# Performance work log

Measured on AMD Instinct MI355X. Metric: run time of the kernel, lower is better.

## Reference

```python
import jax, jax.numpy as jnp
import numpy as np

B, T, DIN, D = 32, 2048, 512, 512


def setup_inputs() -> dict:
    key = jax.random.key(0)
    k0, k1, k2, k3 = jax.random.split(key, 4)
    x = jax.random.normal(k0, (B, T, DIN), dtype=jnp.float32)
    h0 = jax.random.normal(k1, (B, D), dtype=jnp.float32)
    s0 = jax.random.normal(k2, (B, D), dtype=jnp.float32)
    # nn.Linear(input_dim, 6*hidden_dim): weight [6D, DIN], bias [6D]
    W = jax.random.normal(k3, (6 * D, DIN), dtype=jnp.float32) / np.float32(np.sqrt(DIN))
    b = jnp.zeros((6 * D,), dtype=jnp.float32)
    return {"x": x, "h0": h0, "s0": s0, "W": W, "b": b}


def reference(x, h0, s0, W, b):
    # Fused input projection for all 6 gates, done once as a big GEMM: [B,T,6D]
    proj = jnp.einsum("bti,oi->bto", x, W) + b
    proj = jnp.transpose(proj, (1, 0, 2))  # [T, B, 6D] for scan over time
    sig = jax.nn.sigmoid

    def step(carry, z):
        h, s = carry  # each [B, D]
        z0, z1, z2, z3, z4, z5 = jnp.split(z, 6, axis=-1)
        # gated two-state recurrence (6 gates, input-only projection,
        # elementwise recurrence on h/s as in the fused Triton cell)
        s_new = sig(z0) * s + sig(z1) * jnp.tanh(z2)
        h_new = sig(z3) * h + sig(z4) * jnp.tanh(z5 + s_new)
        return (h_new, s_new), h_new

    (hT, sT), hs = jax.lax.scan(step, (h0, s0), proj)
    out = jnp.transpose(hs, (1, 0, 2))  # [B, T, D]
    return out, sT
```

## Files before the change

kernel.cpp:

```cpp
#include <hip/hip_runtime.h>
#include <hip/hip_bf16.h>
#include <cstddef>
#include <cstdint>

#define BB   32
#define TT   2048
#define DIN  512
#define DD   512
#define NN   3072
#define PW   3072
#define PF   16

#define BMT 256
#define BNT 256
#define BKT 64
#define NKT (DIN / BKT)

typedef __attribute__((ext_vector_type(4))) float f32x4;
typedef __attribute__((ext_vector_type(8))) short s16x8;

__device__ __forceinline__ void gl2lds16(const void* g, void* l) {
    __builtin_amdgcn_global_load_lds(
        (const __attribute__((address_space(1))) unsigned*)g,
        (__attribute__((address_space(3))) unsigned*)l, 16, 0, 0);
}

__device__ __forceinline__ unsigned short bfr(float f) {
    unsigned u = __float_as_uint(f);
    u += 0x7fffu + ((u >> 16) & 1u);
    return (unsigned short)(u >> 16);
}

__device__ __forceinline__ float ftanh(float x) {
    return 1.f - 2.f * __builtin_amdgcn_rcpf(1.f + __builtin_amdgcn_exp2f(x * 2.885390082f));
}

__device__ __forceinline__ float h2lo(unsigned u) {
    return (float)__builtin_bit_cast(_Float16, (unsigned short)(u & 0xffffu));
}
__device__ __forceinline__ float h2hi(unsigned u) {
    return (float)__builtin_bit_cast(_Float16, (unsigned short)(u >> 16));
}

__global__ __launch_bounds__(256) void convert_x(
    const float* __restrict__ x, unsigned short* __restrict__ x2)
{
    const int total4 = BB * TT * DIN / 4;
    for (int idx = blockIdx.x * 256 + threadIdx.x; idx < total4;
         idx += gridDim.x * 256) {
        int e = idx * 4;
        int b = e >> 20;
        int t = (e >> 9) & 2047;
        int i = e & 511;
        float4 v = *(const float4*)(x + (size_t)e);
        ushort4 o;
        o.x = bfr(v.x); o.y = bfr(v.y); o.z = bfr(v.z); o.w = bfr(v.w);
        *(ushort4*)(x2 + ((size_t)((t << 5) | b) << 9) + i) = o;
    }
}

__global__ __launch_bounds__(128) void convert_w(
    const float* __restrict__ W, const float* __restrict__ bias,
    unsigned short* __restrict__ W2, float* __restrict__ bias2)
{
    int c = blockIdx.x;
    int p = c >> 10, d = (c & 1023) >> 1, q = c & 1;
    int o = ((2 * p + q) << 9) + d;
    const float* src = W + (size_t)o * DIN;
    unsigned short* dst = W2 + (size_t)c * DIN;
    int i = threadIdx.x * 4;
    float4 v = *(const float4*)(src + i);
    ushort4 u;
    u.x = bfr(v.x); u.y = bfr(v.y); u.z = bfr(v.z); u.w = bfr(v.w);
    *(ushort4*)(dst + i) = u;
    if (threadIdx.x == 0) bias2[c] = bias[o];
}

__global__ __launch_bounds__(512, 2) void gemm_proj8(
    const unsigned short* __restrict__ x2,
    const unsigned short* __restrict__ W2,
    const float* __restrict__ bias2,
    _Float16* __restrict__ proj,
    int t0)
{
    __shared__ unsigned short lds[4 * 256 * 64];
    unsigned short* const A0 = lds;
    unsigned short* const B0 = lds + 16384;
    unsigned short* const A1 = lds + 32768;
    unsigned short* const B1 = lds + 49152;

    const int tid  = threadIdx.x;
    const int bx   = blockIdx.x % (NN / BNT);
    const int by   = blockIdx.x / (NN / BNT);
    const int row0 = by * BMT;
    const int col0 = bx * BNT;
    const size_t growA = (size_t)t0 * BB + row0;

    const int lane = tid & 63;
    const int wv   = tid >> 6;
    const int wm   = wv >> 2;
    const int wn   = wv & 3;
    const int lr   = lane & 15;
    const int lq   = lane >> 4;

    auto stage = [&](unsigned short* Ab, unsigned short* Bb, int kt) {
        const int k0 = kt * BKT;
        #pragma unroll
        for (int a = 0; a < 4; ++a) {
            int cid = a * 512 + tid;
            int rt  = cid >> 3;
            int cp  = cid & 7;
            int cl  = cp ^ (rt & 7);
            gl2lds16(x2 + (growA + rt) * DIN + k0 + cl * 8, Ab + rt * 64 + cp * 8);
        }
        #pragma unroll
        for (int a = 0; a < 4; ++a) {
            int cid = a * 512 + tid;
            int rt  = cid >> 3;
            int cp  = cid & 7;
            int cl  = cp ^ (rt & 7);
            gl2lds16(W2 + (size_t)(col0 + rt) * DIN + k0 + cl * 8, Bb + rt * 64 + cp * 8);
        }
    };

    f32x4 acc[8][4] = {};

    stage(A0, B0, 0);
    stage(A1, B1, 1);
    asm volatile("s_waitcnt vmcnt(8)" ::: "memory");
    __builtin_amdgcn_s_barrier();

    #pragma unroll
    for (int kt = 0; kt < NKT; ++kt) {
        const unsigned short* Ab = (kt & 1) ? A1 : A0;
        const unsigned short* Bb = (kt & 1) ? B1 : B0;

        s16x8 bv[4][2];
        #pragma unroll
        for (int j = 0; j < 4; ++j) {
            int col = wn * 64 + j * 16 + lr;
            #pragma unroll
            for (int x = 0; x < 2; ++x) {
                int cp = (x * 4 + lq) ^ (col & 7);
                bv[j][x] = *(const s16x8*)(Bb + col * 64 + cp * 8);
            }
        }
        #pragma unroll
        for (int m = 0; m < 8; ++m) {
            int row = wm * 128 + m * 16 + lr;
            s16x8 av0, av1;
            {
                int cp0 = (0 * 4 + lq) ^ (row & 7);
                int cp1 = (1 * 4 + lq) ^ (row & 7);
                av0 = *(const s16x8*)(Ab + row * 64 + cp0 * 8);
                av1 = *(const s16x8*)(Ab + row * 64 + cp1 * 8);
            }
            __builtin_amdgcn_s_setprio(1);
            #pragma unroll
            for (int j = 0; j < 4; ++j) {
                acc[m][j] = __builtin_amdgcn_mfma_f32_16x16x32_bf16(
                    av0, bv[j][0], acc[m][j], 0, 0, 0);
                acc[m][j] = __builtin_amdgcn_mfma_f32_16x16x32_bf16(
                    av1, bv[j][1], acc[m][j], 0, 0, 0);
            }
            __builtin_amdgcn_s_setprio(0);
        }

        __builtin_amdgcn_s_barrier();
        if (kt + 2 < NKT) {
            stage((kt & 1) ? A1 : A0, (kt & 1) ? B1 : B0, kt + 2);
            asm volatile("s_waitcnt vmcnt(8)" ::: "memory");
        } else if (kt + 1 < NKT) {
            asm volatile("s_waitcnt vmcnt(0)" ::: "memory");
        }
        if (kt + 1 < NKT) __builtin_amdgcn_s_barrier();
    }

    #pragma unroll
    for (int j = 0; j < 4; ++j) {
        int col = col0 + wn * 64 + j * 16 + lr;
        int p   = col >> 10;
        int q   = col & 1;
        int k   = 2 * p + q;
        float bc = bias2[col];
        const bool  isT = (k == 2);
        const bool  isI = (k == 5);
        const float m   = isT ? 2.885390082f : -1.442695041f;
        #pragma unroll
        for (int i = 0; i < 8; ++i) {
            int rbase = row0 + wm * 128 + i * 16 + lq * 4;
            #pragma unroll
            for (int r = 0; r < 4; ++r) {
                float z  = acc[i][j][r] + bc;
                float e  = __builtin_amdgcn_exp2f(z * m);
                float rr = __builtin_amdgcn_rcpf(1.f + e);
                float v  = isT ? (1.f - 2.f * rr) : rr;
                if (isI) v = z;
                proj[(size_t)(rbase + r) * PW + col] = (_Float16)v;
            }
        }
    }
}

__global__ __launch_bounds__(64) void scan_chunk(
    const _Float16* __restrict__ proj,
    const float* __restrict__ h0, const float* __restrict__ s0,
    float* __restrict__ outH, float* __restrict__ outS,
    int t0, int Tc)
{
    const int gid = blockIdx.x * 64 + threadIdx.x;
    const int b   = gid >> 9;
    const int d   = gid & 511;

    float h, s;
    if (t0 == 0) { h = h0[gid]; s = s0[gid]; }
    else {
        h = outH[((size_t)b * TT + (t0 - 1)) * DD + d];
        s = outS[gid];
    }

    const unsigned* pu = (const unsigned*)(proj + (size_t)b * PW + d * 2);
    const size_t tstr = (size_t)BB * PW / 2;
    float* oH = outH + ((size_t)b * TT + t0) * DD + d;

    unsigned bufA[PF][3], bufB[PF][3];
    #pragma unroll
    for (int u = 0; u < PF; ++u)
        #pragma unroll
        for (int p = 0; p < 3; ++p)
            bufA[u][p] = pu[(size_t)u * tstr + p * 512];

    for (int tb = 0; tb < Tc; tb += 2 * PF) {
        #pragma unroll
        for (int u = 0; u < PF; ++u) {
            int t = tb + PF + u; if (t > Tc - 1) t = Tc - 1;
            #pragma unroll
            for (int p = 0; p < 3; ++p)
                bufB[u][p] = pu[(size_t)t * tstr + p * 512];
        }
        #pragma unroll
        for (int u = 0; u < PF; ++u) {
            float a0 = h2lo(bufA[u][0]), a1 = h2hi(bufA[u][0]);
            float t2 = h2lo(bufA[u][1]), a3 = h2hi(bufA[u][1]);
            float a4 = h2lo(bufA[u][2]), z5 = h2hi(bufA[u][2]);
            s = __builtin_fmaf(a0, s, a1 * t2);
            h = __builtin_fmaf(a3, h, a4 * ftanh(z5 + s));
            oH[(size_t)(tb + u) * DD] = h;
        }
        #pragma unroll
        for (int u = 0; u < PF; ++u) {
            int t = tb + 2 * PF + u; if (t > Tc - 1) t = Tc - 1;
            #pragma unroll
            for (int p = 0; p < 3; ++p)
                bufA[u][p] = pu[(size_t)t * tstr + p * 512];
        }
        #pragma unroll
        for (int u = 0; u < PF; ++u) {
            float a0 = h2lo(bufB[u][0]), a1 = h2hi(bufB[u][0]);
            float t2 = h2lo(bufB[u][1]), a3 = h2hi(bufB[u][1]);
            float a4 = h2lo(bufB[u][2]), z5 = h2hi(bufB[u][2]);
            s = __builtin_fmaf(a0, s, a1 * t2);
            h = __builtin_fmaf(a3, h, a4 * ftanh(z5 + s));
            oH[(size_t)(tb + PF + u) * DD] = h;
        }
    }

    outS[gid] = s;
}

extern "C" void kernel_launch(void* const* d_in, const int* in_sizes, int n_in,
                              void* d_out, int out_size, void* d_ws, size_t ws_size,
                              hipStream_t stream) {
    const float* x    = (const float*)d_in[0];
    const float* h0   = (const float*)d_in[1];
    const float* s0   = (const float*)d_in[2];
    const float* W    = (const float*)d_in[3];
    const float* bias = (const float*)d_in[4];

    float* outH = (float*)d_out;
    float* outS = outH + (size_t)BB * TT * DD;

    char* ws = (char*)d_ws;
    const size_t x2_bytes = (size_t)BB * TT * DIN * 2;
    const size_t w2_bytes = (size_t)NN * DIN * 2;
    const size_t b2_bytes = (size_t)NN * 4;
    unsigned short* x2    = (unsigned short*)ws;
    unsigned short* W2    = (unsigned short*)(ws + x2_bytes);
    float*          bias2 = (float*)(ws + x2_bytes + w2_bytes);
    _Float16*       proj  = (_Float16*)(ws + x2_bytes + w2_bytes + b2_bytes);

    const size_t fixed = x2_bytes + w2_bytes + b2_bytes;
    const size_t per_t = (size_t)BB * PW * 2;
    size_t avail = ws_size > fixed ? ws_size - fixed : 0;
    int TcMax = (int)(avail / per_t);
    if (TcMax > 512) TcMax = 512;
    TcMax &= ~31;
    if (TcMax < 32) TcMax = 32;

    convert_x<<<2048, 256, 0, stream>>>(x, x2);
    convert_w<<<NN, 128, 0, stream>>>(W, bias, W2, bias2);

    for (int t0 = 0; t0 < TT; t0 += TcMax) {
        int Tc = TT - t0;
        if (Tc > TcMax) Tc = TcMax;
        int nblk = (NN / BNT) * (Tc * BB / BMT);
        gemm_proj8<<<nblk, 512, 0, stream>>>(x2, W2, bias2, proj, t0);
        scan_chunk<<<(BB * DD) / 64, 64, 0, stream>>>(proj, h0, s0, outH, outS, t0, Tc);
    }
}
```

Baseline: 486.6 us.

## Remap GEMM workgroups per XCD, split A/B staging, vectorize transposed epilogue stores

Blocks are remapped so that consecutive output tiles land on the same XCD, which should improve L2 reuse of shared x/W tiles. B-tile staging for step k+2 is now issued right after the B fragments are read into registers, and A staging still waits until after the MFMA loop, so loads overlap compute sooner. The MFMA operands are swapped so each lane holds four consecutive columns, which lets the epilogue write ushort4 vector stores with a vectorized bias load and per-tile gate selection. The trade-offs are an extra barrier and lgkmcnt waits per k-step, and the epilogue relies on the column permutation parity.

```diff
diff --git a/kernel.cpp b/kernel.cpp
--- a/kernel.cpp
+++ b/kernel.cpp
@@ -84,14 +84,19 @@
     int t0)
 {
     __shared__ unsigned short lds[4 * 256 * 64];
-    unsigned short* const A0 = lds;
-    unsigned short* const B0 = lds + 16384;
-    unsigned short* const A1 = lds + 32768;
-    unsigned short* const B1 = lds + 49152;
+    unsigned short* const Abuf[2] = { lds,          lds + 32768 };
+    unsigned short* const Bbuf[2] = { lds + 16384,  lds + 49152 };
+
+    const unsigned nwg = gridDim.x;
+    const unsigned fb  = blockIdx.x;
+    const unsigned qq  = nwg >> 3, rr8 = nwg & 7;
+    const unsigned xcd = fb & 7, sid = fb >> 3;
+    const unsigned work = (xcd < rr8 ? xcd * (qq + 1)
+                                     : rr8 * (qq + 1) + (xcd - rr8) * qq) + sid;
+    const int bx = (int)(work % (NN / BNT));
+    const int by = (int)(work / (NN / BNT));
 
     const int tid  = threadIdx.x;
-    const int bx   = blockIdx.x % (NN / BNT);
-    const int by   = blockIdx.x / (NN / BNT);
     const int row0 = by * BMT;
     const int col0 = bx * BNT;
     const size_t growA = (size_t)t0 * BB + row0;
@@ -103,7 +108,7 @@
     const int lr   = lane & 15;
     const int lq   = lane >> 4;
 
-    auto stage = [&](unsigned short* Ab, unsigned short* Bb, int kt) {
+    auto stageA = [&](unsigned short* Ab, int kt) {
         const int k0 = kt * BKT;
         #pragma unroll
         for (int a = 0; a < 4; ++a) {
@@ -113,6 +118,9 @@
             int cl  = cp ^ (rt & 7);
             gl2lds16(x2 + (growA + rt) * DIN + k0 + cl * 8, Ab + rt * 64 + cp * 8);
         }
+    };
+    auto stageB = [&](unsigned short* Bb, int kt) {
+        const int k0 = kt * BKT;
         #pragma unroll
         for (int a = 0; a < 4; ++a) {
             int cid = a * 512 + tid;
@@ -125,15 +133,15 @@
 
     f32x4 acc[8][4] = {};
 
-    stage(A0, B0, 0);
-    stage(A1, B1, 1);
+    stageA(Abuf[0], 0); stageB(Bbuf[0], 0);
+    stageA(Abuf[1], 1); stageB(Bbuf[1], 1);
     asm volatile("s_waitcnt vmcnt(8)" ::: "memory");
     __builtin_amdgcn_s_barrier();
 
     #pragma unroll
     for (int kt = 0; kt < NKT; ++kt) {
-        const unsigned short* Ab = (kt & 1) ? A1 : A0;
-        const unsigned short* Bb = (kt & 1) ? B1 : B0;
+        const unsigned short* Ab = Abuf[kt & 1];
+        const unsigned short* Bb = Bbuf[kt & 1];
 
         s16x8 bv[4][2];
         #pragma unroll
@@ -145,30 +153,34 @@
                 bv[j][x] = *(const s16x8*)(Bb + col * 64 + cp * 8);
             }
         }
+        asm volatile("s_waitcnt lgkmcnt(0)" ::: "memory");
+        __builtin_amdgcn_sched_barrier(0);
+        __builtin_amdgcn_s_barrier();
+        if (kt + 2 < NKT) stageB(Bbuf[kt & 1], kt + 2);
+
         #pragma unroll
         for (int m = 0; m < 8; ++m) {
             int row = wm * 128 + m * 16 + lr;
-            s16x8 av0, av1;
-            {
-                int cp0 = (0 * 4 + lq) ^ (row & 7);
-                int cp1 = (1 * 4 + lq) ^ (row & 7);
-                av0 = *(const s16x8*)(Ab + row * 64 + cp0 * 8);
-                av1 = *(const s16x8*)(Ab + row * 64 + cp1 * 8);
-            }
+            int cp0 = (lq)     ^ (row & 7);
+            int cp1 = (4 + lq) ^ (row & 7);
+            s16x8 av0 = *(const s16x8*)(Ab + row * 64 + cp0 * 8);
+            s16x8 av1 = *(const s16x8*)(Ab + row * 64 + cp1 * 8);
             __builtin_amdgcn_s_setprio(1);
             #pragma unroll
             for (int j = 0; j < 4; ++j) {
                 acc[m][j] = __builtin_amdgcn_mfma_f32_16x16x32_bf16(
-                    av0, bv[j][0], acc[m][j], 0, 0, 0);
+                    bv[j][0], av0, acc[m][j], 0, 0, 0);
                 acc[m][j] = __builtin_amdgcn_mfma_f32_16x16x32_bf16(
-                    av1, bv[j][1], acc[m][j], 0, 0, 0);
+                    bv[j][1], av1, acc[m][j], 0, 0, 0);
             }
             __builtin_amdgcn_s_setprio(0);
         }
-
+        asm volatile("s_waitcnt lgkmcnt(0)" ::: "memory");
+        __builtin_amdgcn_sched_barrier(0);
         __builtin_amdgcn_s_barrier();
+
         if (kt + 2 < NKT) {
-            stage((kt & 1) ? A1 : A0, (kt & 1) ? B1 : B0, kt + 2);
+            stageA(Abuf[kt & 1], kt + 2);
             asm volatile("s_waitcnt vmcnt(8)" ::: "memory");
         } else if (kt + 1 < NKT) {
             asm volatile("s_waitcnt vmcnt(0)" ::: "memory");
@@ -176,28 +188,37 @@
         if (kt + 1 < NKT) __builtin_amdgcn_s_barrier();
     }
 
+    const int p = col0 >> 10;
+    const bool evenTanh = (p == 1);
+    const bool oddIdent = (p == 2);
+    const float mEven = evenTanh ? 2.885390082f : -1.442695041f;
+
     #pragma unroll
-    for (int j = 0; j < 4; ++j) {
-        int col = col0 + wn * 64 + j * 16 + lr;
-        int p   = col >> 10;
-        int q   = col & 1;
-        int k   = 2 * p + q;
-        float bc = bias2[col];
-        const bool  isT = (k == 2);
-        const bool  isI = (k == 5);
-        const float m   = isT ? 2.885390082f : -1.442695041f;
-        #pragma unroll
-        for (int i = 0; i < 8; ++i) {
-            int rbase = row0 + wm * 128 + i * 16 + lq * 4;
-            #pragma unroll
-            for (int r = 0; r < 4; ++r) {
-                float z  = acc[i][j][r] + bc;
-                float e  = __builtin_amdgcn_exp2f(z * m);
-                float rr = __builtin_amdgcn_rcpf(1.f + e);
-                float v  = isT ? (1.f - 2.f * rr) : rr;
-                if (isI) v = z;
-                proj[(size_t)(rbase + r) * PW + col] = (_Float16)v;
-            }
+    for (int m = 0; m < 8; ++m) {
+        int prow = row0 + wm * 128 + m * 16 + lr;
+        _Float16* dst = proj + (size_t)prow * PW;
+        #pragma unroll
+        for (int j = 0; j < 4; ++j) {
+            int cbase = col0 + wn * 64 + j * 16 + lq * 4;
+            float4 bc = *(const float4*)(bias2 + cbase);
+            float z0 = acc[m][j][0] + bc.x;
+            float z1 = acc[m][j][1] + bc.y;
+            float z2 = acc[m][j][2] + bc.z;
+            float z3 = acc[m][j][3] + bc.w;
+            float e0 = __builtin_amdgcn_rcpf(1.f + __builtin_amdgcn_exp2f(z0 * mEven));
+            float e2 = __builtin_amdgcn_rcpf(1.f + __builtin_amdgcn_exp2f(z2 * mEven));
+            float v0 = evenTanh ? (1.f - 2.f * e0) : e0;
+            float v2 = evenTanh ? (1.f - 2.f * e2) : e2;
+            float v1 = oddIdent ? z1
+                : __builtin_amdgcn_rcpf(1.f + __builtin_amdgcn_exp2f(z1 * -1.442695041f));
+            float v3 = oddIdent ? z3
+                : __builtin_amdgcn_rcpf(1.f + __builtin_amdgcn_exp2f(z3 * -1.442695041f));
+            ushort4 o;
+            o.x = __builtin_bit_cast(unsigned short, (_Float16)v0);
+            o.y = __builtin_bit_cast(unsigned short, (_Float16)v1);
+            o.z = __builtin_bit_cast(unsigned short, (_Float16)v2);
+            o.w = __builtin_bit_cast(unsigned short, (_Float16)v3);
+            *(ushort4*)(dst + cbase) = o;
         }
     }
 }
```

Result: no change. 492.1 us (+1.1%).
